# Performance work log

Hardware: AMD Instinct MI355X
Metric: run time of the kernel (lower is better)

## Reference

```python
import jax, jax.numpy as jnp
import numpy as np

DIM, HEADS = 512, 8
HD = DIM // HEADS
B, T = 1, 512


def _rope_tables(T, hd):
    inv_freq = 1.0 / (10000.0 ** (jnp.arange(0, hd, 2, dtype=jnp.float32) / hd))
    freqs = jnp.arange(T, dtype=jnp.float32)[:, None] * inv_freq[None, :]
    emb = jnp.concatenate([freqs, freqs], axis=-1)  # [T, hd]
    return jnp.cos(emb), jnp.sin(emb)


def _rotate_half_heads(x):
    # Faithful to source: torch chunk(2, dim=1) on [B,H,hd,1,T] splits the HEADS axis.
    x1, x2 = jnp.split(x, 2, axis=1)
    return jnp.concatenate([-x2, x1], axis=1)


def setup_inputs():
    key = jax.random.key(0)
    ks = jax.random.split(key, 5)
    s = 1.0 / np.sqrt(DIM)
    return {
        "x": jax.random.normal(ks[0], (B, T, DIM), dtype=jnp.float32),
        "Wq": jax.random.normal(ks[1], (DIM, DIM), dtype=jnp.float32) * s,
        "Wk": jax.random.normal(ks[2], (DIM, DIM), dtype=jnp.float32) * s,
        "Wv": jax.random.normal(ks[3], (DIM, DIM), dtype=jnp.float32) * s,
        "Wo": jax.random.normal(ks[4], (DIM, DIM), dtype=jnp.float32) * s,
    }


def reference(x, Wq, Wk, Wv, Wo):
    b, t, d = x.shape
    h, hd = HEADS, d // HEADS
    scale = 1.0 / np.sqrt(hd)

    def proj(W):
        # 1x1 Conv2d == per-position linear; channel o = head*hd + c  -> [B,H,hd,T]
        return jnp.einsum('btd,od->bot', x, W).reshape(b, h, hd, t)

    q, k, v = proj(Wq), proj(Wk), proj(Wv)

    cos, sin = _rope_tables(t, hd)
    cosT = cos.T[None, None]  # [1,1,hd,T]
    sinT = sin.T[None, None]
    q = q * cosT + _rotate_half_heads(q) * sinT
    k = k * cosT + _rotate_half_heads(k) * sinT

    # Per-channel outer-product scores (inner dim of the matmul is the singleton axis)
    att = jnp.einsum('bhci,bhcj->bhcij', q, k) * scale  # [B,H,hd,T,T]
    causal_mask = jnp.triu(jnp.ones((t, t), dtype=bool), k=1)
    att = jnp.where(causal_mask, -jnp.inf, att)
    att = jax.nn.softmax(att, axis=-1)

    out = jnp.einsum('bhcij,bhcj->bhci', att, v).reshape(b, d, t)
    return jnp.einsum('od,bdt->bto', Wo, out)  # [B,T,D]
```

## Files before the change

kernel.cpp:

```cpp
#include <hip/hip_runtime.h>
#include <math.h>

typedef __attribute__((ext_vector_type(8))) short short8;
typedef __attribute__((ext_vector_type(4))) float floatx4;

__device__ __forceinline__ unsigned short f2bf(float f) {
    unsigned int u = __builtin_bit_cast(unsigned int, f);
    u += 0x7FFFu + ((u >> 16) & 1u);
    return (unsigned short)(u >> 16);
}


__global__ __launch_bounds__(256) void cvt_bf16(
    const float* __restrict__ x,  const float* __restrict__ Wq,
    const float* __restrict__ Wk, const float* __restrict__ Wv,
    const float* __restrict__ Wo, unsigned short* __restrict__ Wallb,
    unsigned short* __restrict__ xb, unsigned short* __restrict__ Wob)
{
    const float* src; unsigned short* dst;
    switch (blockIdx.y) {
        case 0: src = Wq; dst = Wallb;          break;
        case 1: src = Wk; dst = Wallb + 262144; break;
        case 2: src = Wv; dst = Wallb + 524288; break;
        case 3: src = x;  dst = xb;             break;
        default: src = Wo; dst = Wob;           break;
    }
    const int i4 = (blockIdx.x * 256 + threadIdx.x) * 4;
    const float4 v = *(const float4*)(src + i4);
    ushort4 o;
    o.x = f2bf(v.x); o.y = f2bf(v.y); o.z = f2bf(v.z); o.w = f2bf(v.w);
    *(ushort4*)(dst + i4) = o;
}

__global__ __launch_bounds__(256) void gemm_bt(
    const unsigned short* __restrict__ A,
    const unsigned short* __restrict__ B,
    float* __restrict__ C)
{
    __shared__ unsigned short As[64 * 64];
    __shared__ unsigned short Bs[64 * 64];

    const int tid  = threadIdx.x;
    const int lane = tid & 63;
    const int w    = tid >> 6;
    const int m0   = blockIdx.y * 64;
    const int n0   = blockIdx.x * 64;
    const int wm   = (w >> 1) * 32;
    const int wn   = (w & 1) * 32;

    const int srow8 = w * 8 + (lane >> 3);
    const int c8    = lane & 7;

    floatx4 acc[2][2] = {{{0.f,0.f,0.f,0.f},{0.f,0.f,0.f,0.f}},
                         {{0.f,0.f,0.f,0.f},{0.f,0.f,0.f,0.f}}};

    const int quad = lane >> 4;
    const int l15  = lane & 15;

    for (int kc = 0; kc < 512; kc += 64) {
        #pragma unroll
        for (int rr = 0; rr < 2; ++rr) {
            const int row  = rr * 32 + srow8;
            const int gcol = kc + ((c8 ^ (row & 7)) * 8);
            const unsigned short* ga = A + (m0 + row) * 512 + gcol;
            const unsigned short* gb = B + (n0 + row) * 512 + gcol;
            __builtin_amdgcn_global_load_lds(
                (const __attribute__((address_space(1))) void*)ga,
                (__attribute__((address_space(3))) void*)&As[(rr * 32 + w * 8) * 64],
                16, 0, 0);
            __builtin_amdgcn_global_load_lds(
                (const __attribute__((address_space(1))) void*)gb,
                (__attribute__((address_space(3))) void*)&Bs[(rr * 32 + w * 8) * 64],
                16, 0, 0);
        }
        __syncthreads();

        #pragma unroll
        for (int ks = 0; ks < 2; ++ks) {
            const int cIdx = ks * 4 + quad;
            short8 a[2], b[2];
            #pragma unroll
            for (int mt = 0; mt < 2; ++mt) {
                const int row = wm + mt * 16 + l15;
                a[mt] = *(const short8*)&As[row * 64 + ((cIdx ^ (row & 7)) * 8)];
            }
            #pragma unroll
            for (int nt = 0; nt < 2; ++nt) {
                const int row = wn + nt * 16 + l15;
                b[nt] = *(const short8*)&Bs[row * 64 + ((cIdx ^ (row & 7)) * 8)];
            }
            #pragma unroll
            for (int mt = 0; mt < 2; ++mt)
                #pragma unroll
                for (int nt = 0; nt < 2; ++nt)
                    acc[mt][nt] = __builtin_amdgcn_mfma_f32_16x16x32_bf16(
                        a[mt], b[nt], acc[mt][nt], 0, 0, 0);
        }
        __syncthreads();
    }

    #pragma unroll
    for (int mt = 0; mt < 2; ++mt)
        #pragma unroll
        for (int nt = 0; nt < 2; ++nt) {
            const int grow = m0 + wm + mt * 16 + quad * 4;
            const int gcol = n0 + wn + nt * 16 + l15;
            #pragma unroll
            for (int r = 0; r < 4; ++r)
                C[(grow + r) * 512 + gcol] = acc[mt][nt][r];
        }
}

__global__ __launch_bounds__(512) void attn_rope(
    const float* __restrict__ qkv, float* __restrict__ att)
{
    const int ch = blockIdx.x;
    const int i  = threadIdx.x;
    const int c  = ch & 63;
    const int p  = ch ^ 256;
    const float sgn = (ch < 256) ? -1.f : 1.f;

    __shared__ float ks_[512];
    __shared__ float vs_[512];

    const float* __restrict__ qg = qkv;
    const float* __restrict__ kg = qkv + 262144;
    const float* __restrict__ vg = qkv + 524288;

    const float inv_freq = powf(10000.f, -(float)(c & 31) * (1.f / 32.f));
    float sn, cs;
    sincosf((float)i * inv_freq, &sn, &cs);

    const float kv = kg[ch * 512 + i], kpv = kg[p * 512 + i];
    ks_[i] = (kv * cs + sgn * kpv * sn) * 0.125f;
    vs_[i] = vg[ch * 512 + i];
    const float qv = qg[ch * 512 + i], qpv = qg[p * 512 + i];
    const float qi = qv * cs + sgn * qpv * sn;
    __syncthreads();

    float l = 0.f, acc = 0.f;
    const int jend = i & ~63;

    #pragma unroll 2
    for (int j = 0; j < jend; j += 4) {
        const float4 a4 = *(const float4*)&ks_[j];
        const float4 v4 = *(const float4*)&vs_[j];
        float e;
        e = __expf(qi * a4.x); l += e; acc = fmaf(e, v4.x, acc);
        e = __expf(qi * a4.y); l += e; acc = fmaf(e, v4.y, acc);
        e = __expf(qi * a4.z); l += e; acc = fmaf(e, v4.z, acc);
        e = __expf(qi * a4.w); l += e; acc = fmaf(e, v4.w, acc);
    }
    #pragma unroll
    for (int u = 0; u < 64; u += 4) {
        const int j = jend + u;
        const float4 a4 = *(const float4*)&ks_[j];
        const float4 v4 = *(const float4*)&vs_[j];
        float e;
        e = (j + 0 <= i) ? __expf(qi * a4.x) : 0.f; l += e; acc = fmaf(e, v4.x, acc);
        e = (j + 1 <= i) ? __expf(qi * a4.y) : 0.f; l += e; acc = fmaf(e, v4.y, acc);
        e = (j + 2 <= i) ? __expf(qi * a4.z) : 0.f; l += e; acc = fmaf(e, v4.z, acc);
        e = (j + 3 <= i) ? __expf(qi * a4.w) : 0.f; l += e; acc = fmaf(e, v4.w, acc);
    }
    att[ch * 512 + i] = acc / l;
}

__global__ __launch_bounds__(256) void attT_cvt(
    const float* __restrict__ att, unsigned short* __restrict__ attTb)
{
    __shared__ float tile[32][33];
    const int d0 = blockIdx.y * 32, t0 = blockIdx.x * 32;
    const int tx = threadIdx.x, ty = threadIdx.y;
    #pragma unroll
    for (int i = 0; i < 32; i += 8)
        tile[ty + i][tx] = att[(d0 + ty + i) * 512 + t0 + tx];
    __syncthreads();
    #pragma unroll
    for (int i = 0; i < 32; i += 8)
        attTb[(t0 + ty + i) * 512 + d0 + tx] = f2bf(tile[tx][ty + i]);
}

extern "C" void kernel_launch(void* const* d_in, const int* in_sizes, int n_in,
                              void* d_out, int out_size, void* d_ws, size_t ws_size,
                              hipStream_t stream)
{
    const float* x  = (const float*)d_in[0];
    const float* Wq = (const float*)d_in[1];
    const float* Wk = (const float*)d_in[2];
    const float* Wv = (const float*)d_in[3];
    const float* Wo = (const float*)d_in[4];
    float* out = (float*)d_out;

    unsigned short* Wallb = (unsigned short*)d_ws;
    unsigned short* xb    = Wallb + 786432;
    unsigned short* Wob   = xb + 262144;
    unsigned short* attTb = Wob + 262144;
    float* qkvf = (float*)(attTb + 262144);
    float* attf = qkvf + 786432;

    cvt_bf16<<<dim3(256, 5), 256, 0, stream>>>(x, Wq, Wk, Wv, Wo, Wallb, xb, Wob);
    gemm_bt<<<dim3(8, 24), 256, 0, stream>>>(Wallb, xb, qkvf);
    attn_rope<<<512, 512, 0, stream>>>(qkvf, attf);
    attT_cvt<<<dim3(16, 16), dim3(32, 8), 0, stream>>>(attf, attTb);
    gemm_bt<<<dim3(8, 8), 256, 0, stream>>>(attTb, Wob, out);
}
```

Baseline: 104.0 us.

## Double-buffer GEMM LDS, pair causal rows, fuse transpose into attention

The GEMM now double-buffers its LDS tiles with async global-to-LDS loads and explicit vmcnt waits, so the next tile's load overlaps the current tile's MFMAs. The attention kernel gives each thread a pair of rows (t and 511-t) to balance causal work, and switches to exp2 with the log2(e) factor folded into the scale. It also writes a transposed bf16 result directly, which removes the separate transpose/convert kernel and one fp32 round trip. Risks include strided 2-byte transposed stores and higher register pressure from two accumulators per thread.

```diff
diff --git a/kernel.cpp b/kernel.cpp
--- a/kernel.cpp
+++ b/kernel.cpp
@@ -37,8 +37,8 @@
     const unsigned short* __restrict__ B,
     float* __restrict__ C)
 {
-    __shared__ unsigned short As[64 * 64];
-    __shared__ unsigned short Bs[64 * 64];
+    __shared__ unsigned short As[2][64 * 64];
+    __shared__ unsigned short Bs[2][64 * 64];
 
     const int tid  = threadIdx.x;
     const int lane = tid & 63;
@@ -57,7 +57,7 @@
     const int quad = lane >> 4;
     const int l15  = lane & 15;
 
-    for (int kc = 0; kc < 512; kc += 64) {
+    auto stage = [&](int kc, int buf) {
         #pragma unroll
         for (int rr = 0; rr < 2; ++rr) {
             const int row  = rr * 32 + srow8;
@@ -66,14 +66,28 @@
             const unsigned short* gb = B + (n0 + row) * 512 + gcol;
             __builtin_amdgcn_global_load_lds(
                 (const __attribute__((address_space(1))) void*)ga,
-                (__attribute__((address_space(3))) void*)&As[(rr * 32 + w * 8) * 64],
+                (__attribute__((address_space(3))) void*)&As[buf][(rr * 32 + w * 8) * 64],
                 16, 0, 0);
             __builtin_amdgcn_global_load_lds(
                 (const __attribute__((address_space(1))) void*)gb,
-                (__attribute__((address_space(3))) void*)&Bs[(rr * 32 + w * 8) * 64],
+                (__attribute__((address_space(3))) void*)&Bs[buf][(rr * 32 + w * 8) * 64],
                 16, 0, 0);
         }
-        __syncthreads();
+    };
+
+    stage(0, 0);
+
+    #pragma unroll
+    for (int kt = 0; kt < 8; ++kt) {
+        const int cur = kt & 1;
+        if (kt < 7) {
+            stage((kt + 1) * 64, cur ^ 1);
+            asm volatile("s_waitcnt vmcnt(4)" ::: "memory");
+        } else {
+            asm volatile("s_waitcnt vmcnt(0)" ::: "memory");
+        }
+        __builtin_amdgcn_s_barrier();
+        __builtin_amdgcn_sched_barrier(0);
 
         #pragma unroll
         for (int ks = 0; ks < 2; ++ks) {
@@ -82,12 +96,12 @@
             #pragma unroll
             for (int mt = 0; mt < 2; ++mt) {
                 const int row = wm + mt * 16 + l15;
-                a[mt] = *(const short8*)&As[row * 64 + ((cIdx ^ (row & 7)) * 8)];
+                a[mt] = *(const short8*)&As[cur][row * 64 + ((cIdx ^ (row & 7)) * 8)];
             }
             #pragma unroll
             for (int nt = 0; nt < 2; ++nt) {
                 const int row = wn + nt * 16 + l15;
-                b[nt] = *(const short8*)&Bs[row * 64 + ((cIdx ^ (row & 7)) * 8)];
+                b[nt] = *(const short8*)&Bs[cur][row * 64 + ((cIdx ^ (row & 7)) * 8)];
             }
             #pragma unroll
             for (int mt = 0; mt < 2; ++mt)
@@ -96,7 +110,8 @@
                     acc[mt][nt] = __builtin_amdgcn_mfma_f32_16x16x32_bf16(
                         a[mt], b[nt], acc[mt][nt], 0, 0, 0);
         }
-        __syncthreads();
+        __builtin_amdgcn_s_barrier();
+        __builtin_amdgcn_sched_barrier(0);
     }
 
     #pragma unroll
@@ -111,12 +126,13 @@
         }
 }
 
-__global__ __launch_bounds__(512) void attn_rope(
-    const float* __restrict__ qkv, float* __restrict__ att)
+__global__ __launch_bounds__(256) void attn_rope(
+    const float* __restrict__ qkv, unsigned short* __restrict__ attTb)
 {
     const int ch = blockIdx.x;
-    const int i  = threadIdx.x;
-    const int c  = ch & 63;
+    const int t  = threadIdx.x;
+    const int i1 = t;
+    const int i2 = 511 - t;
     const int p  = ch ^ 256;
     const float sgn = (ch < 256) ? -1.f : 1.f;
 
@@ -127,57 +143,79 @@
     const float* __restrict__ kg = qkv + 262144;
     const float* __restrict__ vg = qkv + 524288;
 
-    const float inv_freq = powf(10000.f, -(float)(c & 31) * (1.f / 32.f));
-    float sn, cs;
-    sincosf((float)i * inv_freq, &sn, &cs);
-
-    const float kv = kg[ch * 512 + i], kpv = kg[p * 512 + i];
-    ks_[i] = (kv * cs + sgn * kpv * sn) * 0.125f;
-    vs_[i] = vg[ch * 512 + i];
-    const float qv = qg[ch * 512 + i], qpv = qg[p * 512 + i];
-    const float qi = qv * cs + sgn * qpv * sn;
+    const float inv_freq = powf(10000.f, -(float)(ch & 31) * (1.f / 32.f));
+    const float SC = 0.125f * 1.44269504088896f;
+
+    float sn_a, cs_a, sn_b, cs_b, sn_c, cs_c;
+    sincosf((float)t * inv_freq,         &sn_a, &cs_a);
+    sincosf((float)(t + 256) * inv_freq, &sn_b, &cs_b);
+    sincosf((float)i2 * inv_freq,        &sn_c, &cs_c);
+
+    ks_[t]       = (kg[ch * 512 + t]       * cs_a + sgn * kg[p * 512 + t]       * sn_a) * SC;
+    ks_[t + 256] = (kg[ch * 512 + t + 256] * cs_b + sgn * kg[p * 512 + t + 256] * sn_b) * SC;
+    vs_[t]       = vg[ch * 512 + t];
+    vs_[t + 256] = vg[ch * 512 + t + 256];
+    const float q1 = qg[ch * 512 + i1] * cs_a + sgn * qg[p * 512 + i1] * sn_a;
+    const float q2 = qg[ch * 512 + i2] * cs_c + sgn * qg[p * 512 + i2] * sn_c;
     __syncthreads();
 
-    float l = 0.f, acc = 0.f;
-    const int jend = i & ~63;
+    float l1 = 0.f, a1 = 0.f, l2 = 0.f, a2 = 0.f;
+    const int w64 = t & ~63;
 
     #pragma unroll 2
-    for (int j = 0; j < jend; j += 4) {
-        const float4 a4 = *(const float4*)&ks_[j];
-        const float4 v4 = *(const float4*)&vs_[j];
-        float e;
-        e = __expf(qi * a4.x); l += e; acc = fmaf(e, v4.x, acc);
-        e = __expf(qi * a4.y); l += e; acc = fmaf(e, v4.y, acc);
-        e = __expf(qi * a4.z); l += e; acc = fmaf(e, v4.z, acc);
-        e = __expf(qi * a4.w); l += e; acc = fmaf(e, v4.w, acc);
-    }
-    #pragma unroll
+    for (int j = 0; j < w64; j += 4) {
+        const float4 kk = *(const float4*)&ks_[j];
+        const float4 vv = *(const float4*)&vs_[j];
+        float e;
+        e = __builtin_amdgcn_exp2f(q1 * kk.x); l1 += e; a1 = fmaf(e, vv.x, a1);
+        e = __builtin_amdgcn_exp2f(q2 * kk.x); l2 += e; a2 = fmaf(e, vv.x, a2);
+        e = __builtin_amdgcn_exp2f(q1 * kk.y); l1 += e; a1 = fmaf(e, vv.y, a1);
+        e = __builtin_amdgcn_exp2f(q2 * kk.y); l2 += e; a2 = fmaf(e, vv.y, a2);
+        e = __builtin_amdgcn_exp2f(q1 * kk.z); l1 += e; a1 = fmaf(e, vv.z, a1);
+        e = __builtin_amdgcn_exp2f(q2 * kk.z); l2 += e; a2 = fmaf(e, vv.z, a2);
+        e = __builtin_amdgcn_exp2f(q1 * kk.w); l1 += e; a1 = fmaf(e, vv.w, a1);
+        e = __builtin_amdgcn_exp2f(q2 * kk.w); l2 += e; a2 = fmaf(e, vv.w, a2);
+    }
+    #pragma unroll 4
     for (int u = 0; u < 64; u += 4) {
-        const int j = jend + u;
-        const float4 a4 = *(const float4*)&ks_[j];
-        const float4 v4 = *(const float4*)&vs_[j];
-        float e;
-        e = (j + 0 <= i) ? __expf(qi * a4.x) : 0.f; l += e; acc = fmaf(e, v4.x, acc);
-        e = (j + 1 <= i) ? __expf(qi * a4.y) : 0.f; l += e; acc = fmaf(e, v4.y, acc);
-        e = (j + 2 <= i) ? __expf(qi * a4.z) : 0.f; l += e; acc = fmaf(e, v4.z, acc);
-        e = (j + 3 <= i) ? __expf(qi * a4.w) : 0.f; l += e; acc = fmaf(e, v4.w, acc);
-    }
-    att[ch * 512 + i] = acc / l;
-}
-
-__global__ __launch_bounds__(256) void attT_cvt(
-    const float* __restrict__ att, unsigned short* __restrict__ attTb)
-{
-    __shared__ float tile[32][33];
-    const int d0 = blockIdx.y * 32, t0 = blockIdx.x * 32;
-    const int tx = threadIdx.x, ty = threadIdx.y;
-    #pragma unroll
-    for (int i = 0; i < 32; i += 8)
-        tile[ty + i][tx] = att[(d0 + ty + i) * 512 + t0 + tx];
-    __syncthreads();
-    #pragma unroll
-    for (int i = 0; i < 32; i += 8)
-        attTb[(t0 + ty + i) * 512 + d0 + tx] = f2bf(tile[tx][ty + i]);
+        const int j = w64 + u;
+        const float4 kk = *(const float4*)&ks_[j];
+        const float4 vv = *(const float4*)&vs_[j];
+        float e;
+        e = (j + 0 <= i1) ? __builtin_amdgcn_exp2f(q1 * kk.x) : 0.f; l1 += e; a1 = fmaf(e, vv.x, a1);
+        e = __builtin_amdgcn_exp2f(q2 * kk.x);                       l2 += e; a2 = fmaf(e, vv.x, a2);
+        e = (j + 1 <= i1) ? __builtin_amdgcn_exp2f(q1 * kk.y) : 0.f; l1 += e; a1 = fmaf(e, vv.y, a1);
+        e = __builtin_amdgcn_exp2f(q2 * kk.y);                       l2 += e; a2 = fmaf(e, vv.y, a2);
+        e = (j + 2 <= i1) ? __builtin_amdgcn_exp2f(q1 * kk.z) : 0.f; l1 += e; a1 = fmaf(e, vv.z, a1);
+        e = __builtin_amdgcn_exp2f(q2 * kk.z);                       l2 += e; a2 = fmaf(e, vv.z, a2);
+        e = (j + 3 <= i1) ? __builtin_amdgcn_exp2f(q1 * kk.w) : 0.f; l1 += e; a1 = fmaf(e, vv.w, a1);
+        e = __builtin_amdgcn_exp2f(q2 * kk.w);                       l2 += e; a2 = fmaf(e, vv.w, a2);
+    }
+    const int jend2 = 448 - w64;
+    #pragma unroll 2
+    for (int j = w64 + 64; j < jend2; j += 4) {
+        const float4 kk = *(const float4*)&ks_[j];
+        const float4 vv = *(const float4*)&vs_[j];
+        float e;
+        e = __builtin_amdgcn_exp2f(q2 * kk.x); l2 += e; a2 = fmaf(e, vv.x, a2);
+        e = __builtin_amdgcn_exp2f(q2 * kk.y); l2 += e; a2 = fmaf(e, vv.y, a2);
+        e = __builtin_amdgcn_exp2f(q2 * kk.z); l2 += e; a2 = fmaf(e, vv.z, a2);
+        e = __builtin_amdgcn_exp2f(q2 * kk.w); l2 += e; a2 = fmaf(e, vv.w, a2);
+    }
+    #pragma unroll 4
+    for (int u = 0; u < 64; u += 4) {
+        const int j = jend2 + u;
+        const float4 kk = *(const float4*)&ks_[j];
+        const float4 vv = *(const float4*)&vs_[j];
+        float e;
+        e = (j + 0 <= i2) ? __builtin_amdgcn_exp2f(q2 * kk.x) : 0.f; l2 += e; a2 = fmaf(e, vv.x, a2);
+        e = (j + 1 <= i2) ? __builtin_amdgcn_exp2f(q2 * kk.y) : 0.f; l2 += e; a2 = fmaf(e, vv.y, a2);
+        e = (j + 2 <= i2) ? __builtin_amdgcn_exp2f(q2 * kk.z) : 0.f; l2 += e; a2 = fmaf(e, vv.z, a2);
+        e = (j + 3 <= i2) ? __builtin_amdgcn_exp2f(q2 * kk.w) : 0.f; l2 += e; a2 = fmaf(e, vv.w, a2);
+    }
+
+    attTb[i1 * 512 + ch] = f2bf(a1 / l1);
+    attTb[i2 * 512 + ch] = f2bf(a2 / l2);
 }
 
 extern "C" void kernel_launch(void* const* d_in, const int* in_sizes, int n_in,
@@ -196,11 +234,9 @@
     unsigned short* Wob   = xb + 262144;
     unsigned short* attTb = Wob + 262144;
     float* qkvf = (float*)(attTb + 262144);
-    float* attf = qkvf + 786432;
 
     cvt_bf16<<<dim3(256, 5), 256, 0, stream>>>(x, Wq, Wk, Wv, Wo, Wallb, xb, Wob);
     gemm_bt<<<dim3(8, 24), 256, 0, stream>>>(Wallb, xb, qkvf);
-    attn_rope<<<512, 512, 0, stream>>>(qkvf, attf);
-    attT_cvt<<<dim3(16, 16), dim3(32, 8), 0, stream>>>(attf, attTb);
+    attn_rope<<<512, 256, 0, stream>>>(qkvf, attTb);
     gemm_bt<<<dim3(8, 8), 256, 0, stream>>>(attTb, Wob, out);
 }
```

Result: faster. 93.68 us (-9.9%).
